# Kernel optimization log

Measured on AMD Instinct MI355X. Metric: run time of the kernel, lower is better.

The kernel has to match this reference:

```python
import jax, jax.numpy as jnp
from jax import lax
import numpy as np

# ----- static optical constants (from config) -----
N = 500            # phase mask grid
PX = 1e-6          # pixel pitch [m]
WL = 532e-9        # wavelength [m]
FL = 0.1           # focal length [m]
RI = 1.0           # refractive index
FWHC = 150e-6      # laser beam FWHC
K = 2.0 * np.pi * RI / WL
QE, DARK_MEAN, READ_STD, GAIN, MAX_ADU = 0.9, 0.005, 1.6, 2.0, 65535.0
MAX_VAL = 4.0e9    # Normalize01 max
PHOTONS = 1.0e6    # photons per emitter (max_intensity-style scaling)
R = 15             # psf_keep_radius -> 31x31 crops

_x = np.arange(-N // 2, N // 2) * PX
_X, _Y = np.meshgrid(_x, _x)
INCIDENT = np.exp(-(_X**2 + _Y**2) / (2.0 * FWHC**2)).astype(np.float32)
_C1 = (np.pi / (WL * FL) * (_X**2 + _Y**2)) % (2.0 * np.pi)
B1 = np.exp(-1j * _C1).astype(np.complex64)
# angular-spectrum gamma, directly in unshifted fft order
_F = np.fft.fftfreq(N, d=PX)
_A, _B = np.meshgrid(RI * WL * _F, RI * WL * _F)
GAMMA = np.sqrt(np.maximum(1.0 - _A**2 - _B**2, 0.0)).astype(np.float32)

def _gauss7():
    m = (7 - 1) / 2.0
    y, x = np.ogrid[-m:m + 1, -m:m + 1]
    h = np.exp(-(x * x + y * y) / 2.0)
    h[h < np.finfo(h.dtype).eps * h.max()] = 0
    return h.astype(np.float32)
GAUSS7 = _gauss7()


def setup_inputs() -> dict:
    key = jax.random.key(0)
    k1, k2, k3, k4, k5, k6, k7 = jax.random.split(key, 7)
    B, Ne = 8, 64
    phase_mask = jax.random.uniform(k1, (N, N), jnp.float32, 0.0, 2.0 * np.pi)
    zs = jax.random.uniform(k2, (Ne,), jnp.float32, 0.0, 1e-4)  # defocus depths [m]
    xyz = jax.random.randint(k3, (B, Ne, 2), 0, 170, jnp.int32) + 15  # in [15,184]
    std_u = jax.random.uniform(k4, (1,), jnp.float32)
    eps_dark = jax.random.normal(k5, (B, 1, 198, 198), jnp.float32)
    eps_photon = jax.random.normal(k6, (B, 1, 198, 198), jnp.float32)
    eps_read = jax.random.normal(k7, (B, 1, 198, 198), jnp.float32)
    return {"phase_mask": phase_mask, "zs": zs, "xyz": xyz, "std_u": std_u,
            "eps_dark": eps_dark, "eps_photon": eps_photon, "eps_read": eps_read}


def _forward(phase_mask, zs, xyz, std_u, eps_dark, eps_photon, eps_read):
    Bn, Ne = xyz.shape[0], xyz.shape[1]
    # --- FFT-based PSF generation (angular spectrum propagation) ---
    field = (INCIDENT * jnp.exp(1j * phase_mask) * B1).astype(jnp.complex64)  # [N,N]
    Ef = jnp.fft.fft2(field)                                                  # [N,N]
    H = jnp.exp(1j * ((K * GAMMA)[None] * zs[:, None, None]))                 # [Ne,N,N]
    Eprop = jnp.fft.ifft2(Ef[None] * H)                                       # [Ne,N,N]
    inten = jnp.abs(Eprop) ** 2
    c = N // 2
    psf = inten[:, c - R:c + R + 1, c - R:c + R + 1]                          # [Ne,31,31]
    psf = psf / (jnp.sum(psf, (-2, -1), keepdims=True) + 1e-12) * PHOTONS
    images4D = jnp.broadcast_to(psf[None], (Bn, Ne, 2 * R + 1, 2 * R + 1))
    # --- imgs4dto3d: scatter-add 31x31 patches into 200x200 canvas ---
    offs = jnp.arange(2 * R + 1) - R
    rows = xyz[..., 0][..., None, None] + offs[None, None, :, None]           # [B,Ne,31,1]
    cols = xyz[..., 1][..., None, None] + offs[None, None, None, :]           # [B,Ne,1,31]
    bidx = jnp.arange(Bn)[:, None, None, None]
    canvas = jnp.zeros((Bn, 200, 200), psf.dtype).at[bidx, rows, cols].add(images4D)
    img = canvas[:, None]                                                     # [B,1,200,200]
    # --- BlurLayer: per-draw std gaussian, conv pad=2 -> 198x198 ---
    std = 0.8 + 0.4 * std_u[0]
    s2 = std * std
    kern = (1.0 / (2.0 * jnp.pi * s2)) * GAUSS7 ** (1.0 / s2)
    blurred = lax.conv_general_dilated(img, kern[None, None], (1, 1),
                                       [(2, 2), (2, 2)],
                                       dimension_numbers=("NCHW", "OIHW", "NCHW"))
    # --- NoiseLayer (reparameterized gaussian approximations) ---
    sig = blurred * QE
    dark = DARK_MEAN + eps_dark * jnp.sqrt(jnp.float32(DARK_MEAN))
    total = jnp.maximum(sig + dark, 0.0)
    noisy = total + eps_photon * jnp.sqrt(jnp.maximum(total, 1e-12))
    elec = noisy + eps_read * READ_STD
    adu = jnp.clip(elec * GAIN, 0.0, MAX_ADU)
    # --- Normalize01 ---
    out = jnp.where(adu <= 10.0, 1.0, jnp.minimum(adu, MAX_VAL)) / MAX_VAL
    return out.astype(jnp.float32)


def reference(phase_mask, zs, xyz, std_u, eps_dark, eps_photon, eps_read):
    return _forward(phase_mask, zs, xyz, std_u, eps_dark, eps_photon, eps_read)
```

## Files before the change

### kernel.cpp

```cpp
#include <hip/hip_runtime.h>
#include <math.h>

#define NN 500
#define NE 64
#define BATCH 8
#define RR 15
#define PW 31
#define CAN 200
#define OHW 198
#define TWO_PI_F 6.28318530717958647692f
#define SETUP_N (BATCH * CAN * CAN + NE + 49)

#define BCH 16
#define BKC 64
#define BSTR 72
#define BG_CHUNK (2 * 64 * BSTR)
#define ASCALE (1.0f / 64.0f)

using f16x8 = __attribute__((ext_vector_type(8))) _Float16;
using f32x16 = __attribute__((ext_vector_type(16))) float;

__device__ __forceinline__ void fast_sincos_red(float theta, float* s, float* c) {
    const float INV2PI = 0.15915494309189535f;
    const float PI2_HI = 6.28318548202514648f;
    const float PI2_LO = -1.7484556e-7f;
    float n = rintf(theta * INV2PI);
    float r = fmaf(n, -PI2_HI, theta);
    r = fmaf(n, -PI2_LO, r);
    *s = __sinf(r);
    *c = __cosf(r);
}

__global__ void k_setup(const float* __restrict__ std_u,
                        float* __restrict__ kgamma,
                        float2* __restrict__ tw,
                        float* __restrict__ kern,
                        float* __restrict__ canvas,
                        float* __restrict__ psf_sums,
                        _Float16* __restrict__ Bg) {
    int idx = blockIdx.x * blockDim.x + threadIdx.x;
    if (idx < NN) {
        double th = 2.0 * M_PI * (double)idx / (double)NN;
        tw[idx] = make_float2((float)cos(th), (float)sin(th));
    }
    if (idx < BCH * 64 * BSTR) {
        int c = idx / (64 * BSTR);
        int rem = idx % (64 * BSTR);
        int nu = rem / BSTR, j = rem % BSTR;
        float hi = 0.f, lo = 0.f;
        int kap = c * BKC + j;
        if (j < BKC && kap < 2 * NN) {
            int u = kap >> 1, p = kap & 1;
            int ri = nu >> 1, q = nu & 1;
            int r = 235 + ri;
            int m = (u * r) % NN;
            double th = 2.0 * M_PI * (double)m / (double)NN;
            double wre = cos(th), wim = sin(th);
            double val = (q == 0) ? ((p == 0) ? wre : -wim)
                                  : ((p == 0) ? wim : wre);
            float x = (float)val;
            _Float16 h = (_Float16)x;
            hi = (float)h;
            lo = x - (float)h;
        }
        size_t base = (size_t)c * BG_CHUNK + (size_t)nu * BSTR + j;
        Bg[base] = (_Float16)hi;
        Bg[base + (size_t)64 * BSTR] = (_Float16)lo;
    }
    if (idx < BATCH * CAN * CAN) canvas[idx] = 0.f;
    if (idx >= BATCH * CAN * CAN && idx < BATCH * CAN * CAN + NE)
        psf_sums[idx - BATCH * CAN * CAN] = 0.f;
    if (idx >= BATCH * CAN * CAN + NE && idx < SETUP_N) {
        int t = idx - (BATCH * CAN * CAN + NE);
        float stdv = 0.8f + 0.4f * std_u[0];
        float s2 = stdv * stdv;
        int a = t / 7 - 3, b = t % 7 - 3;
        float g = (float)exp(-0.5 * (double)(a * a + b * b));
        kern[t] = (1.0f / (2.0f * (float)M_PI * s2)) * powf(g, 1.0f / s2);
    }
    if (idx >= NN * NN) return;
    int i = idx / NN, j = idx % NN;
    double fy = (double)((i < 250) ? i : i - 500) * 2000.0;
    double fx = (double)((j < 250) ? j : j - 500) * 2000.0;
    double a = 5.32e-7 * fx;
    double b = 5.32e-7 * fy;
    double g = 1.0 - a * a - b * b;
    g = (g > 0.0) ? sqrt(g) : 0.0;
    float Kf = (float)(2.0 * M_PI * 1.0 / 5.32e-7);
    kgamma[idx] = Kf * (float)g;
}

__device__ __forceinline__ void ct_dft_stages(const float2* xs, const float2* tts,
                                              float2* S, int t,
                                              float2* out1, float2* out2, int* kout) {
    if (t < 250) {
        int d = t / 25;
        int b = t % 25;
        float2 st = tts[(25 * d) % NN];
        float wr = 1.f, wi = 0.f;
        float Er = 0.f, Ei = 0.f, Or_ = 0.f, Oi = 0.f;
#pragma unroll
        for (int a = 0; a < 20; a += 2) {
            float2 x0 = xs[25 * a + b];
            Er += x0.x * wr - x0.y * wi;
            Ei += x0.x * wi + x0.y * wr;
            float nr = wr * st.x - wi * st.y;
            float ni = wr * st.y + wi * st.x;
            float2 x1 = xs[25 * (a + 1) + b];
            Or_ += x1.x * nr - x1.y * ni;
            Oi  += x1.x * ni + x1.y * nr;
            wr = nr * st.x - ni * st.y;
            wi = nr * st.y + ni * st.x;
        }
        S[b * 21 + d]      = make_float2(Er + Or_, Ei + Oi);
        S[b * 21 + d + 10] = make_float2(Er - Or_, Ei - Oi);
    }
    __syncthreads();
    if (t < 250) {
        int k = t;
        int d1 = k % 20;
        int d2 = (d1 + 10) % 20;
        float2 s1 = tts[k];
        float wr = 1.f, wi = 0.f;
        float a1r = 0.f, a1i = 0.f, a2r = 0.f, a2i = 0.f;
#pragma unroll
        for (int b = 0; b < 25; ++b) {
            float2 u1 = S[b * 21 + d1];
            float2 u2 = S[b * 21 + d2];
            a1r += u1.x * wr - u1.y * wi;
            a1i += u1.x * wi + u1.y * wr;
            float sgnb = (b & 1) ? -1.f : 1.f;
            float w2r = sgnb * wr, w2i = sgnb * wi;
            a2r += u2.x * w2r - u2.y * w2i;
            a2i += u2.x * w2i + u2.y * w2r;
            float nr = wr * s1.x - wi * s1.y;
            wi = wr * s1.y + wi * s1.x;
            wr = nr;
        }
        *out1 = make_float2(a1r, a1i);
        *out2 = make_float2(a2r, a2i);
        *kout = k;
    }
}

__global__ void k_dft_rows(const float* __restrict__ phase, float2* __restrict__ dst,
                           const float2* __restrict__ tw) {
    __shared__ __align__(16) float2 xs[NN];
    __shared__ float2 tts[NN];
    __shared__ float2 S[25 * 21];
    int line = blockIdx.x;
    int t = threadIdx.x;
    const float INV2SIG = 2.2222222e7f;
    const float C1M = (float)(M_PI / 5.32e-8);
    float y = (float)(line - 250) * 1e-6f;
    float y2 = y * y;
    const float* prow = phase + (size_t)line * NN;
    for (int n = t; n < NN; n += 256) {
        float x = (float)(n - 250) * 1e-6f;
        float r2 = x * x + y2;
        float inc = __expf(-r2 * INV2SIG);
        float c1 = C1M * r2;
        float b1r = __cosf(c1), b1i = -__sinf(c1);
        float ph = prow[n];
        float sp = __sinf(ph), cp = __cosf(ph);
        float ar = inc * cp, ai = inc * sp;
        xs[n] = make_float2(ar * b1r - ai * b1i, ar * b1i + ai * b1r);
        float2 tt = tw[n];
        tts[n] = make_float2(tt.x, -tt.y);
    }
    __syncthreads();
    float2 o1, o2; int k;
    ct_dft_stages(xs, tts, S, t, &o1, &o2, &k);
    if (t < 250) {
        dst[(size_t)k * NN + line] = o1;
        dst[(size_t)(k + 250) * NN + line] = o2;
    }
}

__global__ void k_dft_cols(const float2* __restrict__ src, float2* __restrict__ dst,
                           const float2* __restrict__ tw) {
    __shared__ __align__(16) float2 xs[NN];
    __shared__ float2 tts[NN];
    __shared__ float2 S[25 * 21];
    int line = blockIdx.x;
    const float2* s = src + (size_t)line * NN;
    int t = threadIdx.x;
    for (int n = t; n < NN; n += 256) {
        xs[n] = s[n];
        float2 tt = tw[n];
        tts[n] = make_float2(tt.x, -tt.y);
    }
    __syncthreads();
    float2 o1, o2; int k;
    ct_dft_stages(xs, tts, S, t, &o1, &o2, &k);
    if (t < 250) {
        float2* dp = dst + (size_t)line * NN;
        dp[k] = o1;
        dp[k + 250] = o2;
    }
}

__global__ void __launch_bounds__(256, 3)
k_prop_mfma(const float2* __restrict__ EfT,
            const float* __restrict__ kgamma,
            const float* __restrict__ zs,
            const _Float16* __restrict__ Bg,
            float* __restrict__ part) {
    __shared__ __align__(16) char smem[2 * BG_CHUNK * 2 + 512 * 8 + 512 * 4];
    _Float16* Bbuf = (_Float16*)smem;
    float2*   eft  = (float2*)(smem + 2 * BG_CHUNK * 2);
    float*    kgs  = (float*)(smem + 2 * BG_CHUNK * 2 + 512 * 8);
    float*    ctile = (float*)smem;

    int v = blockIdx.x;
    int t = threadIdx.x;
    int w = t >> 6;
    int wh = w >> 1;
    int mw = w & 1;
    int lane = t & 63;
    int l31 = lane & 31;
    int lk = lane >> 5;

    for (int n = t; n < 512; n += 256) {
        if (n < NN) {
            float2 e = EfT[(size_t)v * NN + n];
            eft[n] = make_float2(e.x * ASCALE, e.y * ASCALE);
            kgs[n] = kgamma[(size_t)v * NN + n];
        } else {
            eft[n] = make_float2(0.f, 0.f);
            kgs[n] = 0.f;
        }
    }
    {
        for (int k = 0; k < 9; ++k) {
            int i = t + k * 256;
            int whs = i / 1152, off = i % 1152;
            ((float4*)Bbuf)[i] =
                ((const float4*)(Bg + (size_t)(8 * whs) * BG_CHUNK))[off];
        }
    }
    float zv = zs[mw * 32 + l31];
    __syncthreads();

    f32x16 acc[2] = {};

#define MODSPLIT(ex, ey, kgv, i0) do {                                        \
        float s_, c_;                                                         \
        fast_sincos_red((kgv) * zv, &s_, &c_);                                \
        float yr = (ex) * c_ - (ey) * s_;                                     \
        float yi = (ex) * s_ + (ey) * c_;                                     \
        _Float16 h0 = (_Float16)yr;                                           \
        ah[i0] = h0; al[i0] = (_Float16)(yr - (float)h0);                     \
        _Float16 h1 = (_Float16)yi;                                           \
        ah[i0 + 1] = h1; al[i0 + 1] = (_Float16)(yi - (float)h1);             \
    } while (0)

    const _Float16* Bb = Bbuf + wh * BG_CHUNK;
    for (int ci = 0; ci < 8; ++ci) {
        float4 stg[9];
        if (ci + 1 < 8) {
#pragma unroll
            for (int k = 0; k < 9; ++k) {
                int i = t + k * 256;
                int whs = i / 1152, off = i % 1152;
                stg[k] = ((const float4*)(Bg +
                            (size_t)(8 * whs + ci + 1) * BG_CHUNK))[off];
            }
        }
#pragma unroll
        for (int sl = 0; sl < 4; ++sl) {
            int step = ci * 4 + sl;
            int u0 = wh * 256 + step * 8 + lk * 4;
            f16x8 ah, al;
            {
                float4 e01 = *(const float4*)&eft[u0];
                float4 e23 = *(const float4*)&eft[u0 + 2];
                float4 kg4 = *(const float4*)&kgs[u0];
                MODSPLIT(e01.x, e01.y, kg4.x, 0);
                MODSPLIT(e01.z, e01.w, kg4.y, 2);
                MODSPLIT(e23.x, e23.y, kg4.z, 4);
                MODSPLIT(e23.z, e23.w, kg4.w, 6);
            }
            int koff = sl * 16 + lk * 8;
#pragma unroll
            for (int nt = 0; nt < 2; ++nt) {
                int nu = nt * 32 + l31;
                f16x8 bh = *(const f16x8*)&Bb[nu * BSTR + koff];
                f16x8 bl = *(const f16x8*)&Bb[64 * BSTR + nu * BSTR + koff];
                acc[nt] = __builtin_amdgcn_mfma_f32_32x32x16_f16(ah, bh, acc[nt], 0, 0, 0);
                acc[nt] = __builtin_amdgcn_mfma_f32_32x32x16_f16(al, bh, acc[nt], 0, 0, 0);
                acc[nt] = __builtin_amdgcn_mfma_f32_32x32x16_f16(ah, bl, acc[nt], 0, 0, 0);
            }
        }
        __syncthreads();
        if (ci + 1 < 8) {
#pragma unroll
            for (int k = 0; k < 9; ++k) {
                int i = t + k * 256;
                ((float4*)Bbuf)[i] = stg[k];
            }
        }
        __syncthreads();
    }
#undef MODSPLIT

    if (wh == 0) {
#pragma unroll
        for (int nt = 0; nt < 2; ++nt)
#pragma unroll
            for (int reg = 0; reg < 16; ++reg) {
                int row = (reg & 3) + 8 * (reg >> 2) + 4 * lk;
                ctile[(mw * 32 + row) * 64 + nt * 32 + l31] = acc[nt][reg];
            }
    }
    __syncthreads();
    if (wh == 1) {
#pragma unroll
        for (int nt = 0; nt < 2; ++nt)
#pragma unroll
            for (int reg = 0; reg < 16; ++reg) {
                int row = (reg & 3) + 8 * (reg >> 2) + 4 * lk;
                ctile[(mw * 32 + row) * 64 + nt * 32 + l31] += acc[nt][reg];
            }
    }
    __syncthreads();
#pragma unroll
    for (int p = 0; p < 4; ++p) {
        int idx = p * 256 + t;
        int z = idx >> 4, c4 = idx & 15;
        float4 val = *(const float4*)&ctile[z * 64 + c4 * 4];
        *(float4*)&part[((size_t)z * NN + v) * 64 + c4 * 4] = val;
    }
}

__global__ void k_prop_cols(const float* __restrict__ part,
                            float* __restrict__ psf,
                            float* __restrict__ psf_sums) {
    __shared__ __align__(16) float X2[NN][16];
    int rq = blockIdx.x;
    int z  = blockIdx.y;
    int t  = threadIdx.x;
    const float* p0 = part + ((size_t)z * NN) * 64 + rq * 16;
    for (int i = t; i < NN * 4; i += 256) {
        int v = i >> 2, q4 = i & 3;
        float4 a = *(const float4*)(p0 + (size_t)v * 64 + q4 * 4);
        *(float4*)&X2[v][q4 * 4] = a;
    }
    __syncthreads();
    int ril = t >> 5;
    int ri  = rq * 8 + ril;
    int ci  = t & 31;
    float val = 0.f;
    if (ri < PW && ci < PW) {
        int c = 235 + ci;
        float ar = 0.f, ai = 0.f;
        float sr, si;
        {
            float th = (TWO_PI_F / NN) * (float)(c % NN);
            sincosf(th, &si, &sr);
        }
        for (int vb = 0; vb < 4; ++vb) {
            int v0 = vb * 125;
            float wr, wi;
            float th = (TWO_PI_F / NN) * (float)((v0 * c) % NN);
            sincosf(th, &wi, &wr);
            for (int v = v0; v < v0 + 125; ++v) {
                float2 xy = *(const float2*)&X2[v][2 * ril];
                ar += xy.x * wr - xy.y * wi;
                ai += xy.x * wi + xy.y * wr;
                float nwr = wr * sr - wi * si;
                wi = wr * si + wi * sr;
                wr = nwr;
            }
        }
        const float inv = 64.0f / 250000.0f;
        float re = ar * inv, im = ai * inv;
        val = re * re + im * im;
        psf[(size_t)z * (PW * PW) + ri * PW + ci] = val;
    }
#pragma unroll
    for (int m = 1; m < 64; m <<= 1) val += __shfl_xor(val, m);
    if ((t & 63) == 0) atomicAdd(&psf_sums[z], val);
}

__global__ void k_scatter(const float* __restrict__ psf,
                          const float* __restrict__ psf_sums,
                          const int* __restrict__ xyz,
                          float* __restrict__ canvas) {
    int e = blockIdx.x;
    int b = blockIdx.y;
    int r0 = xyz[(b * NE + e) * 2 + 0] - RR;
    int c0 = xyz[(b * NE + e) * 2 + 1] - RR;
    float sc = 1.0e6f / (psf_sums[e] + 1e-12f);
    float* cb = canvas + (size_t)b * (CAN * CAN);
    for (int p = threadIdx.x; p < PW * PW; p += blockDim.x) {
        int i = p / PW, j = p % PW;
        atomicAdd(cb + (r0 + i) * CAN + (c0 + j), psf[e * PW * PW + p] * sc);
    }
}

__global__ void k_final(const float* __restrict__ canvas,
                        const float* __restrict__ kern,
                        const float* __restrict__ eps_dark,
                        const float* __restrict__ eps_photon,
                        const float* __restrict__ eps_read,
                        float* __restrict__ out) {
    __shared__ float kk[49];
    __shared__ float tile[14][40];
    int b = blockIdx.z;
    int tx = threadIdx.x, ty = threadIdx.y;
    int t = ty * 32 + tx;
    int j0 = blockIdx.x * 32, i0 = blockIdx.y * 8;
    if (t < 49) kk[t] = kern[t];
    const float* cb = canvas + (size_t)b * (CAN * CAN);
    for (int p = t; p < 14 * 38; p += 256) {
        int rr = p / 38, cc = p % 38;
        int gi = i0 + rr - 2, gj = j0 + cc - 2;
        tile[rr][cc] = (gi >= 0 && gi < CAN && gj >= 0 && gj < CAN)
                           ? cb[gi * CAN + gj] : 0.f;
    }
    __syncthreads();
    int i = i0 + ty, j = j0 + tx;
    if (i >= OHW || j >= OHW) return;
    float acc = 0.f;
#pragma unroll
    for (int a = 0; a < 7; ++a)
#pragma unroll
        for (int q = 0; q < 7; ++q)
            acc += tile[ty + a][tx + q] * kk[a * 7 + q];
    int idx = b * (OHW * OHW) + i * OHW + j;
    float sig = acc * 0.9f;
    float dark = 0.005f + eps_dark[idx] * sqrtf(0.005f);
    float total = fmaxf(sig + dark, 0.0f);
    float noisy = total + eps_photon[idx] * sqrtf(fmaxf(total, 1e-12f));
    float elec = noisy + eps_read[idx] * 1.6f;
    float adu = fminf(fmaxf(elec * 2.0f, 0.0f), 65535.0f);
    float v = (adu <= 10.0f) ? 1.0f : fminf(adu, 4.0e9f);
    out[idx] = v / 4.0e9f;
}

extern "C" void kernel_launch(void* const* d_in, const int* in_sizes, int n_in,
                              void* d_out, int out_size, void* d_ws, size_t ws_size,
                              hipStream_t stream) {
    const float* phase    = (const float*)d_in[0];
    const float* zs       = (const float*)d_in[1];
    const int*   xyz      = (const int*)d_in[2];
    const float* std_u    = (const float*)d_in[3];
    const float* epsd     = (const float*)d_in[4];
    const float* epsp     = (const float*)d_in[5];
    const float* epsr     = (const float*)d_in[6];
    float* out = (float*)d_out;

    char* ws = (char*)d_ws;
    size_t off = 0;
    auto alloc = [&](size_t bytes) {
        off = (off + 255) & ~(size_t)255;
        size_t o = off; off += bytes; return o;
    };
    float*  kgamma   = (float*) (ws + alloc((size_t)NN * NN * 4));
    float2* tw       = (float2*)(ws + alloc((size_t)NN * 8));
    float2* R1T      = (float2*)(ws + alloc((size_t)NN * NN * 8));
    float2* EfT      = (float2*)(ws + alloc((size_t)NN * NN * 8));
    float*  part     = (float*) (ws + alloc((size_t)NE * NN * 64 * 4));
    float*  psf      = (float*) (ws + alloc((size_t)NE * PW * PW * 4));
    float*  psf_sums = (float*) (ws + alloc((size_t)NE * 4));
    float*  kern     = (float*) (ws + alloc((size_t)64 * 4));
    float*  canvas   = (float*) (ws + alloc((size_t)BATCH * CAN * CAN * 4));
    _Float16* Bg     = (_Float16*)(ws + alloc((size_t)BCH * BG_CHUNK * 2));
    (void)ws_size; (void)n_in; (void)in_sizes; (void)out_size;

    k_setup<<<(SETUP_N + 255) / 256, 256, 0, stream>>>(
        std_u, kgamma, tw, kern, canvas, psf_sums, Bg);
    k_dft_rows<<<NN, 256, 0, stream>>>(phase, R1T, tw);
    k_dft_cols<<<NN, 256, 0, stream>>>(R1T, EfT, tw);
    k_prop_mfma<<<NN, 256, 0, stream>>>(EfT, kgamma, zs, Bg, part);
    k_prop_cols<<<dim3(4, NE), 256, 0, stream>>>(part, psf, psf_sums);
    k_scatter<<<dim3(NE, BATCH), 256, 0, stream>>>(psf, psf_sums, xyz, canvas);
    k_final<<<dim3((OHW + 31) / 32, (OHW + 7) / 8, BATCH), dim3(32, 8), 0, stream>>>(
        canvas, kern, epsd, epsp, epsr, out);
}
```

Before: 164.2 us.

## Prepack DFT B-matrix in MFMA fragment layout and load directly from global

```diff
diff --git a/kernel.cpp b/kernel.cpp
--- a/kernel.cpp
+++ b/kernel.cpp
@@ -11,10 +11,7 @@
 #define TWO_PI_F 6.28318530717958647692f
 #define SETUP_N (BATCH * CAN * CAN + NE + 49)
 
-#define BCH 16
-#define BKC 64
-#define BSTR 72
-#define BG_CHUNK (2 * 64 * BSTR)
+#define BG2_F16 (64 * 2 * 2 * 64 * 8)
 #define ASCALE (1.0f / 64.0f)
 
 using f16x8 = __attribute__((ext_vector_type(8))) _Float16;
@@ -37,19 +34,22 @@
                         float* __restrict__ kern,
                         float* __restrict__ canvas,
                         float* __restrict__ psf_sums,
-                        _Float16* __restrict__ Bg) {
+                        _Float16* __restrict__ Bg2) {
     int idx = blockIdx.x * blockDim.x + threadIdx.x;
     if (idx < NN) {
         double th = 2.0 * M_PI * (double)idx / (double)NN;
         tw[idx] = make_float2((float)cos(th), (float)sin(th));
     }
-    if (idx < BCH * 64 * BSTR) {
-        int c = idx / (64 * BSTR);
-        int rem = idx % (64 * BSTR);
-        int nu = rem / BSTR, j = rem % BSTR;
-        float hi = 0.f, lo = 0.f;
-        int kap = c * BKC + j;
-        if (j < BKC && kap < 2 * NN) {
+    if (idx < BG2_F16) {
+        int e = idx & 7;
+        int lane = (idx >> 3) & 63;
+        int nt = (idx >> 9) & 1;
+        int plane = (idx >> 10) & 1;
+        int gs = idx >> 11;
+        int kap = gs * 16 + (lane >> 5) * 8 + e;
+        int nu = nt * 32 + (lane & 31);
+        float outv = 0.f;
+        if (kap < 2 * NN) {
             int u = kap >> 1, p = kap & 1;
             int ri = nu >> 1, q = nu & 1;
             int r = 235 + ri;
@@ -60,12 +60,9 @@
                                   : ((p == 0) ? wim : wre);
             float x = (float)val;
             _Float16 h = (_Float16)x;
-            hi = (float)h;
-            lo = x - (float)h;
-        }
-        size_t base = (size_t)c * BG_CHUNK + (size_t)nu * BSTR + j;
-        Bg[base] = (_Float16)hi;
-        Bg[base + (size_t)64 * BSTR] = (_Float16)lo;
+            outv = (plane == 0) ? (float)h : (x - (float)h);
+        }
+        Bg2[idx] = (_Float16)outv;
     }
     if (idx < BATCH * CAN * CAN) canvas[idx] = 0.f;
     if (idx >= BATCH * CAN * CAN && idx < BATCH * CAN * CAN + NE)
@@ -200,17 +197,15 @@
     }
 }
 
-__global__ void __launch_bounds__(256, 3)
+__global__ void __launch_bounds__(256)
 k_prop_mfma(const float2* __restrict__ EfT,
             const float* __restrict__ kgamma,
             const float* __restrict__ zs,
-            const _Float16* __restrict__ Bg,
+            const _Float16* __restrict__ Bg2,
             float* __restrict__ part) {
-    __shared__ __align__(16) char smem[2 * BG_CHUNK * 2 + 512 * 8 + 512 * 4];
-    _Float16* Bbuf = (_Float16*)smem;
-    float2*   eft  = (float2*)(smem + 2 * BG_CHUNK * 2);
-    float*    kgs  = (float*)(smem + 2 * BG_CHUNK * 2 + 512 * 8);
-    float*    ctile = (float*)smem;
+    __shared__ __align__(16) float2 eft[512];
+    __shared__ __align__(16) float kgs[512];
+    __shared__ __align__(16) float ctile[64 * 64];
 
     int v = blockIdx.x;
     int t = threadIdx.x;
@@ -229,14 +224,6 @@
         } else {
             eft[n] = make_float2(0.f, 0.f);
             kgs[n] = 0.f;
-        }
-    }
-    {
-        for (int k = 0; k < 9; ++k) {
-            int i = t + k * 256;
-            int whs = i / 1152, off = i % 1152;
-            ((float4*)Bbuf)[i] =
-                ((const float4*)(Bg + (size_t)(8 * whs) * BG_CHUNK))[off];
         }
     }
     float zv = zs[mw * 32 + l31];
@@ -255,52 +242,31 @@
         ah[i0 + 1] = h1; al[i0 + 1] = (_Float16)(yi - (float)h1);             \
     } while (0)
 
-    const _Float16* Bb = Bbuf + wh * BG_CHUNK;
-    for (int ci = 0; ci < 8; ++ci) {
-        float4 stg[9];
-        if (ci + 1 < 8) {
-#pragma unroll
-            for (int k = 0; k < 9; ++k) {
-                int i = t + k * 256;
-                int whs = i / 1152, off = i % 1152;
-                stg[k] = ((const float4*)(Bg +
-                            (size_t)(8 * whs + ci + 1) * BG_CHUNK))[off];
-            }
-        }
-#pragma unroll
-        for (int sl = 0; sl < 4; ++sl) {
-            int step = ci * 4 + sl;
-            int u0 = wh * 256 + step * 8 + lk * 4;
-            f16x8 ah, al;
-            {
-                float4 e01 = *(const float4*)&eft[u0];
-                float4 e23 = *(const float4*)&eft[u0 + 2];
-                float4 kg4 = *(const float4*)&kgs[u0];
-                MODSPLIT(e01.x, e01.y, kg4.x, 0);
-                MODSPLIT(e01.z, e01.w, kg4.y, 2);
-                MODSPLIT(e23.x, e23.y, kg4.z, 4);
-                MODSPLIT(e23.z, e23.w, kg4.w, 6);
-            }
-            int koff = sl * 16 + lk * 8;
-#pragma unroll
-            for (int nt = 0; nt < 2; ++nt) {
-                int nu = nt * 32 + l31;
-                f16x8 bh = *(const f16x8*)&Bb[nu * BSTR + koff];
-                f16x8 bl = *(const f16x8*)&Bb[64 * BSTR + nu * BSTR + koff];
-                acc[nt] = __builtin_amdgcn_mfma_f32_32x32x16_f16(ah, bh, acc[nt], 0, 0, 0);
-                acc[nt] = __builtin_amdgcn_mfma_f32_32x32x16_f16(al, bh, acc[nt], 0, 0, 0);
-                acc[nt] = __builtin_amdgcn_mfma_f32_32x32x16_f16(ah, bl, acc[nt], 0, 0, 0);
-            }
-        }
-        __syncthreads();
-        if (ci + 1 < 8) {
-#pragma unroll
-            for (int k = 0; k < 9; ++k) {
-                int i = t + k * 256;
-                ((float4*)Bbuf)[i] = stg[k];
-            }
-        }
-        __syncthreads();
+    const _Float16* bbase = Bg2 + (size_t)(wh * 32) * 2048 + (size_t)lane * 8;
+#pragma unroll 4
+    for (int s = 0; s < 32; ++s) {
+        const _Float16* bs = bbase + (size_t)s * 2048;
+        f16x8 bh0 = *(const f16x8*)(bs);
+        f16x8 bh1 = *(const f16x8*)(bs + 512);
+        f16x8 bl0 = *(const f16x8*)(bs + 1024);
+        f16x8 bl1 = *(const f16x8*)(bs + 1536);
+        int u0 = wh * 256 + s * 8 + lk * 4;
+        f16x8 ah, al;
+        {
+            float4 e01 = *(const float4*)&eft[u0];
+            float4 e23 = *(const float4*)&eft[u0 + 2];
+            float4 kg4 = *(const float4*)&kgs[u0];
+            MODSPLIT(e01.x, e01.y, kg4.x, 0);
+            MODSPLIT(e01.z, e01.w, kg4.y, 2);
+            MODSPLIT(e23.x, e23.y, kg4.z, 4);
+            MODSPLIT(e23.z, e23.w, kg4.w, 6);
+        }
+        acc[0] = __builtin_amdgcn_mfma_f32_32x32x16_f16(ah, bh0, acc[0], 0, 0, 0);
+        acc[0] = __builtin_amdgcn_mfma_f32_32x32x16_f16(al, bh0, acc[0], 0, 0, 0);
+        acc[0] = __builtin_amdgcn_mfma_f32_32x32x16_f16(ah, bl0, acc[0], 0, 0, 0);
+        acc[1] = __builtin_amdgcn_mfma_f32_32x32x16_f16(ah, bh1, acc[1], 0, 0, 0);
+        acc[1] = __builtin_amdgcn_mfma_f32_32x32x16_f16(al, bh1, acc[1], 0, 0, 0);
+        acc[1] = __builtin_amdgcn_mfma_f32_32x32x16_f16(ah, bl1, acc[1], 0, 0, 0);
     }
 #undef MODSPLIT
 
@@ -466,14 +432,14 @@
     float*  psf_sums = (float*) (ws + alloc((size_t)NE * 4));
     float*  kern     = (float*) (ws + alloc((size_t)64 * 4));
     float*  canvas   = (float*) (ws + alloc((size_t)BATCH * CAN * CAN * 4));
-    _Float16* Bg     = (_Float16*)(ws + alloc((size_t)BCH * BG_CHUNK * 2));
+    _Float16* Bg2    = (_Float16*)(ws + alloc((size_t)BG2_F16 * 2));
     (void)ws_size; (void)n_in; (void)in_sizes; (void)out_size;
 
     k_setup<<<(SETUP_N + 255) / 256, 256, 0, stream>>>(
-        std_u, kgamma, tw, kern, canvas, psf_sums, Bg);
+        std_u, kgamma, tw, kern, canvas, psf_sums, Bg2);
     k_dft_rows<<<NN, 256, 0, stream>>>(phase, R1T, tw);
     k_dft_cols<<<NN, 256, 0, stream>>>(R1T, EfT, tw);
-    k_prop_mfma<<<NN, 256, 0, stream>>>(EfT, kgamma, zs, Bg, part);
+    k_prop_mfma<<<NN, 256, 0, stream>>>(EfT, kgamma, zs, Bg2, part);
     k_prop_cols<<<dim3(4, NE), 256, 0, stream>>>(part, psf, psf_sums);
     k_scatter<<<dim3(NE, BATCH), 256, 0, stream>>>(psf, psf_sums, xyz, canvas);
     k_final<<<dim3((OHW + 31) / 32, (OHW + 7) / 8, BATCH), dim3(32, 8), 0, stream>>>(
```

Measured after the change: 137.4 us. -16.3%, faster.
